# Kernel tuning notes

Measured on AMD Instinct MI355X. Metric: run time of the kernel, lower is better.

The kernel has to match this reference:

```python
import jax, jax.numpy as jnp
import numpy as np

T, B, D, H = 1024, 64, 1024, 30  # seq_len, batch, input_size, hidden_size


def setup_inputs() -> dict:
    key = jax.random.key(0)
    ks = jax.random.split(key, 11)
    sc = 1.0 / np.sqrt(H)  # torch default init scale ~ U(-1/sqrt(H), 1/sqrt(H))
    u = lambda k, shape: jax.random.uniform(k, shape, dtype=jnp.float32, minval=-sc, maxval=sc)
    return {
        "x": jax.random.normal(ks[0], (T, B, D), dtype=jnp.float32),
        "W_ih0": u(ks[1], (4 * H, D)),
        "W_hh0": u(ks[2], (4 * H, H)),
        "b_ih0": u(ks[3], (4 * H,)),
        "b_hh0": u(ks[4], (4 * H,)),
        "W_ih1": u(ks[5], (4 * H, H)),
        "W_hh1": u(ks[6], (4 * H, H)),
        "b_ih1": u(ks[7], (4 * H,)),
        "b_hh1": u(ks[8], (4 * H,)),
        "W_out": u(ks[9], (1, H)),
        "b_out": u(ks[10], (1,)),
    }


def _lstm_layer(xs, Wih, Whh, bih, bhh):
    # xs: [T, B, Din] -> hs: [T, B, H]. PyTorch gate order: i, f, g, o.
    xg = jnp.einsum("tbd,gd->tbg", xs, Wih) + (bih + bhh)  # precompute input projection
    h0 = jnp.zeros((xs.shape[1], H), xs.dtype)
    c0 = jnp.zeros((xs.shape[1], H), xs.dtype)

    def step(carry, xw):
        h, c = carry
        gates = xw + h @ Whh.T  # [B, 4H]
        i, f, g, o = jnp.split(gates, 4, axis=-1)
        c = jax.nn.sigmoid(f) * c + jax.nn.sigmoid(i) * jnp.tanh(g)
        h = jax.nn.sigmoid(o) * jnp.tanh(c)
        return (h, c), h

    _, hs = jax.lax.scan(step, (h0, c0), xg)
    return hs


def reference(x, W_ih0, W_hh0, b_ih0, b_hh0, W_ih1, W_hh1, b_ih1, b_hh1, W_out, b_out):
    h1 = _lstm_layer(x, W_ih0, W_hh0, b_ih0, b_hh0)   # layer 0
    h2 = _lstm_layer(h1, W_ih1, W_hh1, b_ih1, b_hh1)  # layer 1
    return h2 @ W_out.T + b_out  # [T, B, 1]
```

## Files before the change

kernel.cpp:

```cpp
#include <hip/hip_runtime.h>
#include <hip/hip_bf16.h>
#include <cstdint>

#define TT 1024
#define BB 64
#define DD 1024
#define HH 30
#define G4 120
#define KC 16

__device__ __forceinline__ float frcp(float x) { return __builtin_amdgcn_rcpf(x); }
__device__ __forceinline__ float fsig(float x) { return frcp(1.0f + __expf(-x)); }
__device__ __forceinline__ float ftan(float x) {
    return 2.0f * frcp(1.0f + __expf(-2.0f * x)) - 1.0f;
}
__device__ __forceinline__ float bcast(float v, int l) {
    return __int_as_float(__builtin_amdgcn_readlane(__float_as_int(v), l));
}

__global__ void prep_kernel(const float* __restrict__ Wih0,
                            const float* __restrict__ bih0,
                            const float* __restrict__ bhh0,
                            float* __restrict__ Wt0, float* __restrict__ bias0) {
    int idx = blockIdx.x * 256 + threadIdx.x;
    int k = idx >> 7, g = idx & 127;
    Wt0[idx] = (g < G4) ? Wih0[g * DD + k] : 0.0f;
    if (idx < 128) bias0[idx] = (idx < G4) ? (bih0[idx] + bhh0[idx]) : 0.0f;
}

__global__ __launch_bounds__(256) void gemm_xg(
    const float* __restrict__ x, const float* __restrict__ Wt0,
    const float* __restrict__ bias0, float* __restrict__ xgp) {
    __shared__ __align__(16) float xs[KC][136];
    __shared__ __align__(16) float ws[KC][132];
    const int tid = threadIdx.x;
    const int r0 = blockIdx.x * 128;
    const int rg = tid >> 4;
    const int cg = tid & 15;

    const int sr = tid >> 1;
    const int sk = (tid & 1) * 8;
    const int ka = tid >> 5;
    const int ca = (tid & 31) * 4;

    float acc[8][8];
#pragma unroll
    for (int i = 0; i < 8; ++i)
#pragma unroll
        for (int j = 0; j < 8; ++j) acc[i][j] = 0.0f;

    const float* xrow = x + (size_t)(r0 + sr) * DD;
    float4 px0 = *(const float4*)&xrow[sk];
    float4 px1 = *(const float4*)&xrow[sk + 4];
    float4 pw0 = *(const float4*)&Wt0[(size_t)ka * 128 + ca];
    float4 pw1 = *(const float4*)&Wt0[(size_t)(ka + 8) * 128 + ca];

    for (int kc = 0; kc < DD / KC; ++kc) {
        __syncthreads();
        xs[sk + 0][sr] = px0.x; xs[sk + 1][sr] = px0.y;
        xs[sk + 2][sr] = px0.z; xs[sk + 3][sr] = px0.w;
        xs[sk + 4][sr] = px1.x; xs[sk + 5][sr] = px1.y;
        xs[sk + 6][sr] = px1.z; xs[sk + 7][sr] = px1.w;
        *(float4*)&ws[ka][ca]     = pw0;
        *(float4*)&ws[ka + 8][ca] = pw1;
        __syncthreads();

        if (kc + 1 < DD / KC) {
            const int k0 = (kc + 1) * KC;
            px0 = *(const float4*)&xrow[k0 + sk];
            px1 = *(const float4*)&xrow[k0 + sk + 4];
            pw0 = *(const float4*)&Wt0[(size_t)(k0 + ka) * 128 + ca];
            pw1 = *(const float4*)&Wt0[(size_t)(k0 + ka + 8) * 128 + ca];
        }

#pragma unroll
        for (int kk = 0; kk < KC; ++kk) {
            float4 xa = *(const float4*)&xs[kk][rg * 8];
            float4 xb = *(const float4*)&xs[kk][rg * 8 + 4];
            float4 wa = *(const float4*)&ws[kk][cg * 8];
            float4 wb = *(const float4*)&ws[kk][cg * 8 + 4];
            float xr[8] = {xa.x, xa.y, xa.z, xa.w, xb.x, xb.y, xb.z, xb.w};
            float wr[8] = {wa.x, wa.y, wa.z, wa.w, wb.x, wb.y, wb.z, wb.w};
#pragma unroll
            for (int i = 0; i < 8; ++i)
#pragma unroll
                for (int j = 0; j < 8; ++j)
                    acc[i][j] = fmaf(xr[i], wr[j], acc[i][j]);
        }
    }

#pragma unroll
    for (int j = 0; j < 8; ++j) {
        const int g = cg * 8 + j;
        if (g < G4) {
            const int gm = g % 60;
            const int lane = (gm < HH) ? gm : (32 + gm - HH);
            const int slot = g / 60;
            const float bb = bias0[g];
#pragma unroll
            for (int i = 0; i < 8; ++i) {
                const size_t row = r0 + rg * 8 + i;
                xgp[(row * 64 + lane) * 2 + slot] = acc[i][j] + bb;
            }
        }
    }
}

__global__ __launch_bounds__(64, 1) void lstm_rec(
    const float* __restrict__ xgp,
    const float* __restrict__ Whh0, const float* __restrict__ Wih1,
    const float* __restrict__ Whh1, const float* __restrict__ bih1,
    const float* __restrict__ bhh1, float* __restrict__ h2buf) {
    const int l = threadIdx.x;
    const int b = blockIdx.x;
    const int u = l & 31;
    const int half = l >> 5;
    const bool act = (u < HH);
    const int rlo = half * HH + (act ? u : 0);
    const int rhi = 60 + rlo;

    float w0lo[HH], w0hi[HH], wi1lo[HH], wi1hi[HH], wh1lo[HH], wh1hi[HH];
#pragma unroll
    for (int j = 0; j < HH; ++j) {
        w0lo[j]  = act ? Whh0[rlo * HH + j] : 0.0f;
        w0hi[j]  = act ? Whh0[rhi * HH + j] : 0.0f;
        wi1lo[j] = act ? Wih1[rlo * HH + j] : 0.0f;
        wi1hi[j] = act ? Wih1[rhi * HH + j] : 0.0f;
        wh1lo[j] = act ? Whh1[rlo * HH + j] : 0.0f;
        wh1hi[j] = act ? Whh1[rhi * HH + j] : 0.0f;
    }
    const float b1lo = act ? (bih1[rlo] + bhh1[rlo]) : 0.0f;
    const float b1hi = act ? (bih1[rhi] + bhh1[rhi]) : 0.0f;

    float h1 = 0.0f, c1 = 0.0f, h2 = 0.0f, c2 = 0.0f;
    float hb1[HH], hb2[HH];
#pragma unroll
    for (int j = 0; j < HH; ++j) { hb1[j] = 0.0f; hb2[j] = 0.0f; }

    const float2* xgptr = (const float2*)xgp + (size_t)b * 64 + l;
    float2 xq[4];
#pragma unroll
    for (int p = 0; p < 4; ++p) xq[p] = xgptr[(size_t)p * (BB * 64)];

    for (int t = 0; t < TT; t += 4) {
#pragma unroll
        for (int p = 0; p < 4; ++p) {
            const int tc = t + p;
            const float2 xw = xq[p];
            const int tn = (tc + 4 < TT) ? tc + 4 : TT - 1;
            xq[p] = xgptr[(size_t)tn * (BB * 64)];

            float aA = xw.x, aB = 0.0f, bA = xw.y, bB = 0.0f;
#pragma unroll
            for (int j = 0; j < HH; j += 2) {
                aA = fmaf(w0lo[j], hb1[j], aA);
                bA = fmaf(w0hi[j], hb1[j], bA);
                aB = fmaf(w0lo[j + 1], hb1[j + 1], aB);
                bB = fmaf(w0hi[j + 1], hb1[j + 1], bB);
            }
            const float alo = aA + aB, ahi = bA + bB;
            const float plo = __shfl_xor(alo, 32, 64);
            const float phi = __shfl_xor(ahi, 32, 64);

            float zA = b1lo, zB = 0.0f, yA = b1hi, yB = 0.0f;
#pragma unroll
            for (int j = 0; j < HH; j += 2) {
                zA = fmaf(wh1lo[j], hb2[j], zA);
                yA = fmaf(wh1hi[j], hb2[j], yA);
                zB = fmaf(wh1lo[j + 1], hb2[j + 1], zB);
                yB = fmaf(wh1hi[j + 1], hb2[j + 1], yB);
            }

            float ipre = half ? plo : alo;
            float fpre = half ? alo : plo;
            float gpre = half ? phi : ahi;
            float opre = half ? ahi : phi;
            c1 = fsig(fpre) * c1 + fsig(ipre) * ftan(gpre);
            h1 = fsig(opre) * ftan(c1);

#pragma unroll
            for (int j = 0; j < HH; ++j) hb1[j] = bcast(h1, j);

#pragma unroll
            for (int j = 0; j < HH; j += 2) {
                zA = fmaf(wi1lo[j], hb1[j], zA);
                yA = fmaf(wi1hi[j], hb1[j], yA);
                zB = fmaf(wi1lo[j + 1], hb1[j + 1], zB);
                yB = fmaf(wi1hi[j + 1], hb1[j + 1], yB);
            }
            const float zlo = zA + zB, zhi = yA + yB;
            const float qlo = __shfl_xor(zlo, 32, 64);
            const float qhi = __shfl_xor(zhi, 32, 64);

            ipre = half ? qlo : zlo;
            fpre = half ? zlo : qlo;
            gpre = half ? qhi : zhi;
            opre = half ? zhi : qhi;
            c2 = fsig(fpre) * c2 + fsig(ipre) * ftan(gpre);
            h2 = fsig(opre) * ftan(c2);

            if (l < HH) h2buf[((size_t)tc * BB + b) * 32 + l] = h2;

#pragma unroll
            for (int j = 0; j < HH; ++j) hb2[j] = bcast(h2, j);
        }
    }
}

__global__ __launch_bounds__(256) void out_proj(
    const float* __restrict__ h2buf, const float* __restrict__ Wout,
    const float* __restrict__ bout, float* __restrict__ out) {
    __shared__ float wos[32];
    if (threadIdx.x < 32)
        wos[threadIdx.x] = (threadIdx.x < HH) ? Wout[threadIdx.x] : 0.0f;
    __syncthreads();
    const int idx = blockIdx.x * 256 + threadIdx.x;
    const float4* hp = (const float4*)(h2buf + (size_t)idx * 32);
    float s0 = 0.f, s1 = 0.f;
#pragma unroll
    for (int q = 0; q < 8; ++q) {
        float4 h = hp[q];
        s0 = fmaf(h.x, wos[q * 4 + 0], s0);
        s1 = fmaf(h.y, wos[q * 4 + 1], s1);
        s0 = fmaf(h.z, wos[q * 4 + 2], s0);
        s1 = fmaf(h.w, wos[q * 4 + 3], s1);
    }
    out[idx] = s0 + s1 + bout[0];
}

extern "C" void kernel_launch(void* const* d_in, const int* in_sizes, int n_in,
                              void* d_out, int out_size, void* d_ws, size_t ws_size,
                              hipStream_t stream) {
    const float* x    = (const float*)d_in[0];
    const float* Wih0 = (const float*)d_in[1];
    const float* Whh0 = (const float*)d_in[2];
    const float* bih0 = (const float*)d_in[3];
    const float* bhh0 = (const float*)d_in[4];
    const float* Wih1 = (const float*)d_in[5];
    const float* Whh1 = (const float*)d_in[6];
    const float* bih1 = (const float*)d_in[7];
    const float* bhh1 = (const float*)d_in[8];
    const float* Wout = (const float*)d_in[9];
    const float* bout = (const float*)d_in[10];
    float* out = (float*)d_out;

    char* ws = (char*)d_ws;
    float* Wt0   = (float*)ws;
    float* bias0 = (float*)(ws + 512 * 1024);
    float* xgp   = (float*)(ws + 1024 * 1024);
    float* h2buf = (float*)(ws + 36 * 1024 * 1024);

    prep_kernel<<<512, 256, 0, stream>>>(Wih0, bih0, bhh0, Wt0, bias0);
    gemm_xg<<<512, 256, 0, stream>>>(x, Wt0, bias0, xgp);
    lstm_rec<<<BB, 64, 0, stream>>>(xgp, Whh0, Wih1, Whh1, bih1, bhh1, h2buf);
    out_proj<<<256, 256, 0, stream>>>(h2buf, Wout, bout, out);
}
```

Before: 1.206 ms.

## Use split-bf16 MFMA for input GEMM and pipeline LSTM layers across two waves

The fp32 SIMT input-projection GEMM becomes an MFMA bf16x3 scheme, with hi/lo bf16 splits of x and the weights prepacked into MFMA fragment layout, so matrix cores do the large GEMM while keeping near-fp32 accuracy. The recurrent kernel now runs two wavefronts per batch element: wave 0 runs layer 0 and the layer-1 input projection, and wave 1 runs layer 1 one timestep behind, exchanging partial gates through double-buffered shared memory. This shortens the serial per-step critical path at the cost of a __syncthreads every step and some truncation error from the bf16 split of x.

Measured after the change: 1.063 ms. -11.8%, faster.

```diff
diff --git a/kernel.cpp b/kernel.cpp
--- a/kernel.cpp
+++ b/kernel.cpp
@@ -7,7 +7,9 @@
 #define DD 1024
 #define HH 30
 #define G4 120
-#define KC 16
+
+typedef __attribute__((ext_vector_type(8))) short short8;
+typedef __attribute__((ext_vector_type(4))) float float4v;
 
 __device__ __forceinline__ float frcp(float x) { return __builtin_amdgcn_rcpf(x); }
 __device__ __forceinline__ float fsig(float x) { return frcp(1.0f + __expf(-x)); }
@@ -17,193 +19,232 @@
 __device__ __forceinline__ float bcast(float v, int l) {
     return __int_as_float(__builtin_amdgcn_readlane(__float_as_int(v), l));
 }
+__device__ __forceinline__ unsigned short bf16_rne(float f) {
+    unsigned u = __float_as_uint(f);
+    return (unsigned short)((u + 0x7FFFu + ((u >> 16) & 1u)) >> 16);
+}
 
 __global__ void prep_kernel(const float* __restrict__ Wih0,
                             const float* __restrict__ bih0,
                             const float* __restrict__ bhh0,
-                            float* __restrict__ Wt0, float* __restrict__ bias0) {
+                            unsigned short* __restrict__ Bhi,
+                            unsigned short* __restrict__ Blo,
+                            float* __restrict__ bias0) {
     int idx = blockIdx.x * 256 + threadIdx.x;
-    int k = idx >> 7, g = idx & 127;
-    Wt0[idx] = (g < G4) ? Wih0[g * DD + k] : 0.0f;
+    int l  = idx & 63;
+    int kc = (idx >> 6) & 31;
+    int nt = idx >> 11;
+    int n = nt * 16 + (l & 15);
+    int kb = kc * 32 + (l >> 4) * 8;
+    size_t o = (size_t)idx * 8;
+#pragma unroll
+    for (int j = 0; j < 8; ++j) {
+        float wv = (n < G4) ? Wih0[(size_t)n * DD + kb + j] : 0.0f;
+        unsigned short hi = bf16_rne(wv);
+        float fhi = __uint_as_float((unsigned)hi << 16);
+        unsigned short lo = bf16_rne(wv - fhi);
+        Bhi[o + j] = hi;
+        Blo[o + j] = lo;
+    }
     if (idx < 128) bias0[idx] = (idx < G4) ? (bih0[idx] + bhh0[idx]) : 0.0f;
 }
 
 __global__ __launch_bounds__(256) void gemm_xg(
-    const float* __restrict__ x, const float* __restrict__ Wt0,
-    const float* __restrict__ bias0, float* __restrict__ xgp) {
-    __shared__ __align__(16) float xs[KC][136];
-    __shared__ __align__(16) float ws[KC][132];
+    const float* __restrict__ x, const unsigned short* __restrict__ Bhi,
+    const unsigned short* __restrict__ Blo, const float* __restrict__ bias0,
+    float* __restrict__ xgp) {
     const int tid = threadIdx.x;
-    const int r0 = blockIdx.x * 128;
-    const int rg = tid >> 4;
-    const int cg = tid & 15;
-
-    const int sr = tid >> 1;
-    const int sk = (tid & 1) * 8;
-    const int ka = tid >> 5;
-    const int ca = (tid & 31) * 4;
-
-    float acc[8][8];
-#pragma unroll
-    for (int i = 0; i < 8; ++i)
-#pragma unroll
-        for (int j = 0; j < 8; ++j) acc[i][j] = 0.0f;
-
-    const float* xrow = x + (size_t)(r0 + sr) * DD;
-    float4 px0 = *(const float4*)&xrow[sk];
-    float4 px1 = *(const float4*)&xrow[sk + 4];
-    float4 pw0 = *(const float4*)&Wt0[(size_t)ka * 128 + ca];
-    float4 pw1 = *(const float4*)&Wt0[(size_t)(ka + 8) * 128 + ca];
-
-    for (int kc = 0; kc < DD / KC; ++kc) {
-        __syncthreads();
-        xs[sk + 0][sr] = px0.x; xs[sk + 1][sr] = px0.y;
-        xs[sk + 2][sr] = px0.z; xs[sk + 3][sr] = px0.w;
-        xs[sk + 4][sr] = px1.x; xs[sk + 5][sr] = px1.y;
-        xs[sk + 6][sr] = px1.z; xs[sk + 7][sr] = px1.w;
-        *(float4*)&ws[ka][ca]     = pw0;
-        *(float4*)&ws[ka + 8][ca] = pw1;
-        __syncthreads();
-
-        if (kc + 1 < DD / KC) {
-            const int k0 = (kc + 1) * KC;
-            px0 = *(const float4*)&xrow[k0 + sk];
-            px1 = *(const float4*)&xrow[k0 + sk + 4];
-            pw0 = *(const float4*)&Wt0[(size_t)(k0 + ka) * 128 + ca];
-            pw1 = *(const float4*)&Wt0[(size_t)(k0 + ka + 8) * 128 + ca];
-        }
-
-#pragma unroll
-        for (int kk = 0; kk < KC; ++kk) {
-            float4 xa = *(const float4*)&xs[kk][rg * 8];
-            float4 xb = *(const float4*)&xs[kk][rg * 8 + 4];
-            float4 wa = *(const float4*)&ws[kk][cg * 8];
-            float4 wb = *(const float4*)&ws[kk][cg * 8 + 4];
-            float xr[8] = {xa.x, xa.y, xa.z, xa.w, xb.x, xb.y, xb.z, xb.w};
-            float wr[8] = {wa.x, wa.y, wa.z, wa.w, wb.x, wb.y, wb.z, wb.w};
-#pragma unroll
-            for (int i = 0; i < 8; ++i)
-#pragma unroll
-                for (int j = 0; j < 8; ++j)
-                    acc[i][j] = fmaf(xr[i], wr[j], acc[i][j]);
-        }
-    }
-
-#pragma unroll
-    for (int j = 0; j < 8; ++j) {
-        const int g = cg * 8 + j;
+    const int w = tid >> 6;
+    const int l = tid & 63;
+    const int lm = l & 15, lq = l >> 4;
+    const int r0 = blockIdx.x * 128 + w * 32;
+
+    float4v acc[2][8];
+#pragma unroll
+    for (int mt = 0; mt < 2; ++mt)
+#pragma unroll
+        for (int nt = 0; nt < 8; ++nt) acc[mt][nt] = (float4v)0.0f;
+
+    const float* aptr[2];
+    aptr[0] = x + (size_t)(r0 + lm) * DD + lq * 8;
+    aptr[1] = x + (size_t)(r0 + 16 + lm) * DD + lq * 8;
+
+    float4 pa[2][2];
+#pragma unroll
+    for (int mt = 0; mt < 2; ++mt) {
+        pa[mt][0] = *(const float4*)(aptr[mt]);
+        pa[mt][1] = *(const float4*)(aptr[mt] + 4);
+    }
+
+    for (int kc = 0; kc < 32; ++kc) {
+        short8 ahi[2], alo[2];
+#pragma unroll
+        for (int mt = 0; mt < 2; ++mt) {
+            float f[8] = {pa[mt][0].x, pa[mt][0].y, pa[mt][0].z, pa[mt][0].w,
+                          pa[mt][1].x, pa[mt][1].y, pa[mt][1].z, pa[mt][1].w};
+#pragma unroll
+            for (int i = 0; i < 8; ++i) {
+                unsigned ub = __float_as_uint(f[i]);
+                ahi[mt][i] = (short)(ub >> 16);
+                float fr = f[i] - __uint_as_float(ub & 0xFFFF0000u);
+                alo[mt][i] = (short)(__float_as_uint(fr) >> 16);
+            }
+        }
+        if (kc + 1 < 32) {
+            const int ko = (kc + 1) * 32;
+#pragma unroll
+            for (int mt = 0; mt < 2; ++mt) {
+                pa[mt][0] = *(const float4*)(aptr[mt] + ko);
+                pa[mt][1] = *(const float4*)(aptr[mt] + ko + 4);
+            }
+        }
+#pragma unroll
+        for (int nt = 0; nt < 8; ++nt) {
+            const size_t bo = ((size_t)(nt * 32 + kc) * 64 + l) * 8;
+            short8 bh = *(const short8*)(Bhi + bo);
+            short8 bl = *(const short8*)(Blo + bo);
+            acc[0][nt] = __builtin_amdgcn_mfma_f32_16x16x32_bf16(ahi[0], bh, acc[0][nt], 0, 0, 0);
+            acc[1][nt] = __builtin_amdgcn_mfma_f32_16x16x32_bf16(ahi[1], bh, acc[1][nt], 0, 0, 0);
+            acc[0][nt] = __builtin_amdgcn_mfma_f32_16x16x32_bf16(alo[0], bh, acc[0][nt], 0, 0, 0);
+            acc[1][nt] = __builtin_amdgcn_mfma_f32_16x16x32_bf16(alo[1], bh, acc[1][nt], 0, 0, 0);
+            acc[0][nt] = __builtin_amdgcn_mfma_f32_16x16x32_bf16(ahi[0], bl, acc[0][nt], 0, 0, 0);
+            acc[1][nt] = __builtin_amdgcn_mfma_f32_16x16x32_bf16(ahi[1], bl, acc[1][nt], 0, 0, 0);
+        }
+    }
+
+#pragma unroll
+    for (int nt = 0; nt < 8; ++nt) {
+        const int g = nt * 16 + lm;
         if (g < G4) {
             const int gm = g % 60;
-            const int lane = (gm < HH) ? gm : (32 + gm - HH);
+            const int lane_t = (gm < HH) ? gm : (32 + gm - HH);
             const int slot = g / 60;
             const float bb = bias0[g];
 #pragma unroll
-            for (int i = 0; i < 8; ++i) {
-                const size_t row = r0 + rg * 8 + i;
-                xgp[(row * 64 + lane) * 2 + slot] = acc[i][j] + bb;
-            }
-        }
-    }
-}
-
-__global__ __launch_bounds__(64, 1) void lstm_rec(
-    const float* __restrict__ xgp,
-    const float* __restrict__ Whh0, const float* __restrict__ Wih1,
-    const float* __restrict__ Whh1, const float* __restrict__ bih1,
-    const float* __restrict__ bhh1, float* __restrict__ h2buf) {
-    const int l = threadIdx.x;
+            for (int mt = 0; mt < 2; ++mt)
+#pragma unroll
+                for (int i = 0; i < 4; ++i) {
+                    const size_t row = r0 + mt * 16 + lq * 4 + i;
+                    xgp[(row * 64 + lane_t) * 2 + slot] = acc[mt][nt][i] + bb;
+                }
+        }
+    }
+}
+
+__global__ __launch_bounds__(128, 1) void lstm_rec(
+    const float* __restrict__ xgp, const float* __restrict__ Whh0,
+    const float* __restrict__ Wih1, const float* __restrict__ Whh1,
+    const float* __restrict__ bih1, const float* __restrict__ bhh1,
+    float* __restrict__ h2buf) {
+    const int tid = threadIdx.x;
+    const int wv = tid >> 6;
+    const int l = tid & 63;
     const int b = blockIdx.x;
     const int u = l & 31;
     const int half = l >> 5;
-    const bool act = (u < HH);
-    const int rlo = half * HH + (act ? u : 0);
+    const bool al = (u < HH);
+    const int rlo = half * HH + (al ? u : 0);
     const int rhi = 60 + rlo;
 
-    float w0lo[HH], w0hi[HH], wi1lo[HH], wi1hi[HH], wh1lo[HH], wh1hi[HH];
-#pragma unroll
-    for (int j = 0; j < HH; ++j) {
-        w0lo[j]  = act ? Whh0[rlo * HH + j] : 0.0f;
-        w0hi[j]  = act ? Whh0[rhi * HH + j] : 0.0f;
-        wi1lo[j] = act ? Wih1[rlo * HH + j] : 0.0f;
-        wi1hi[j] = act ? Wih1[rhi * HH + j] : 0.0f;
-        wh1lo[j] = act ? Whh1[rlo * HH + j] : 0.0f;
-        wh1hi[j] = act ? Whh1[rhi * HH + j] : 0.0f;
-    }
-    const float b1lo = act ? (bih1[rlo] + bhh1[rlo]) : 0.0f;
-    const float b1hi = act ? (bih1[rhi] + bhh1[rhi]) : 0.0f;
-
-    float h1 = 0.0f, c1 = 0.0f, h2 = 0.0f, c2 = 0.0f;
-    float hb1[HH], hb2[HH];
-#pragma unroll
-    for (int j = 0; j < HH; ++j) { hb1[j] = 0.0f; hb2[j] = 0.0f; }
+    __shared__ float2 pg[2][64];
+
+    float wa[HH], wb[HH], wc[HH], wd[HH];
+    float b1lo = 0.f, b1hi = 0.f;
+    if (wv == 0) {
+#pragma unroll
+        for (int j = 0; j < HH; ++j) {
+            wa[j] = al ? Whh0[rlo * HH + j] : 0.f;
+            wb[j] = al ? Whh0[rhi * HH + j] : 0.f;
+            wc[j] = al ? Wih1[rlo * HH + j] : 0.f;
+            wd[j] = al ? Wih1[rhi * HH + j] : 0.f;
+        }
+        b1lo = al ? (bih1[rlo] + bhh1[rlo]) : 0.f;
+        b1hi = al ? (bih1[rhi] + bhh1[rhi]) : 0.f;
+    } else {
+#pragma unroll
+        for (int j = 0; j < HH; ++j) {
+            wa[j] = al ? Whh1[rlo * HH + j] : 0.f;
+            wb[j] = al ? Whh1[rhi * HH + j] : 0.f;
+            wc[j] = 0.f; wd[j] = 0.f;
+        }
+    }
+
+    float hstate = 0.f, cstate = 0.f;
+    float hb[HH];
+#pragma unroll
+    for (int j = 0; j < HH; ++j) hb[j] = 0.f;
 
     const float2* xgptr = (const float2*)xgp + (size_t)b * 64 + l;
     float2 xq[4];
-#pragma unroll
-    for (int p = 0; p < 4; ++p) xq[p] = xgptr[(size_t)p * (BB * 64)];
-
-    for (int t = 0; t < TT; t += 4) {
-#pragma unroll
-        for (int p = 0; p < 4; ++p) {
-            const int tc = t + p;
-            const float2 xw = xq[p];
-            const int tn = (tc + 4 < TT) ? tc + 4 : TT - 1;
-            xq[p] = xgptr[(size_t)tn * (BB * 64)];
-
-            float aA = xw.x, aB = 0.0f, bA = xw.y, bB = 0.0f;
-#pragma unroll
-            for (int j = 0; j < HH; j += 2) {
-                aA = fmaf(w0lo[j], hb1[j], aA);
-                bA = fmaf(w0hi[j], hb1[j], bA);
-                aB = fmaf(w0lo[j + 1], hb1[j + 1], aB);
-                bB = fmaf(w0hi[j + 1], hb1[j + 1], bB);
-            }
-            const float alo = aA + aB, ahi = bA + bB;
-            const float plo = __shfl_xor(alo, 32, 64);
-            const float phi = __shfl_xor(ahi, 32, 64);
-
-            float zA = b1lo, zB = 0.0f, yA = b1hi, yB = 0.0f;
-#pragma unroll
-            for (int j = 0; j < HH; j += 2) {
-                zA = fmaf(wh1lo[j], hb2[j], zA);
-                yA = fmaf(wh1hi[j], hb2[j], yA);
-                zB = fmaf(wh1lo[j + 1], hb2[j + 1], zB);
-                yB = fmaf(wh1hi[j + 1], hb2[j + 1], yB);
-            }
-
-            float ipre = half ? plo : alo;
-            float fpre = half ? alo : plo;
-            float gpre = half ? phi : ahi;
-            float opre = half ? ahi : phi;
-            c1 = fsig(fpre) * c1 + fsig(ipre) * ftan(gpre);
-            h1 = fsig(opre) * ftan(c1);
-
-#pragma unroll
-            for (int j = 0; j < HH; ++j) hb1[j] = bcast(h1, j);
-
-#pragma unroll
-            for (int j = 0; j < HH; j += 2) {
-                zA = fmaf(wi1lo[j], hb1[j], zA);
-                yA = fmaf(wi1hi[j], hb1[j], yA);
-                zB = fmaf(wi1lo[j + 1], hb1[j + 1], zB);
-                yB = fmaf(wi1hi[j + 1], hb1[j + 1], yB);
-            }
-            const float zlo = zA + zB, zhi = yA + yB;
-            const float qlo = __shfl_xor(zlo, 32, 64);
-            const float qhi = __shfl_xor(zhi, 32, 64);
-
-            ipre = half ? qlo : zlo;
-            fpre = half ? zlo : qlo;
-            gpre = half ? qhi : zhi;
-            opre = half ? zhi : qhi;
-            c2 = fsig(fpre) * c2 + fsig(ipre) * ftan(gpre);
-            h2 = fsig(opre) * ftan(c2);
-
-            if (l < HH) h2buf[((size_t)tc * BB + b) * 32 + l] = h2;
-
-#pragma unroll
-            for (int j = 0; j < HH; ++j) hb2[j] = bcast(h2, j);
-        }
+    if (wv == 0) {
+#pragma unroll
+        for (int p = 0; p < 4; ++p) xq[p] = xgptr[(size_t)p * (BB * 64)];
+    }
+
+    for (int t = 0; t <= TT; ++t) {
+        if (wv == 0) {
+            if (t < TT) {
+                float2 xw = xq[t & 3];
+                const int tn = (t + 4 < TT) ? t + 4 : TT - 1;
+                xq[t & 3] = xgptr[(size_t)tn * (BB * 64)];
+
+                float aA = xw.x, aB = 0.f, cA = xw.y, cB = 0.f;
+#pragma unroll
+                for (int j = 0; j < HH; j += 2) {
+                    aA = fmaf(wa[j], hb[j], aA);
+                    cA = fmaf(wb[j], hb[j], cA);
+                    aB = fmaf(wa[j + 1], hb[j + 1], aB);
+                    cB = fmaf(wb[j + 1], hb[j + 1], cB);
+                }
+                float alo = aA + aB, ahi = cA + cB;
+                float plo = __shfl_xor(alo, 32, 64);
+                float phi = __shfl_xor(ahi, 32, 64);
+                float ipre = half ? plo : alo;
+                float fpre = half ? alo : plo;
+                float gpre = half ? phi : ahi;
+                float opre = half ? ahi : phi;
+                cstate = fsig(fpre) * cstate + fsig(ipre) * ftan(gpre);
+                hstate = fsig(opre) * ftan(cstate);
+#pragma unroll
+                for (int j = 0; j < HH; ++j) hb[j] = bcast(hstate, j);
+
+                float zA = b1lo, zB = 0.f, yA = b1hi, yB = 0.f;
+#pragma unroll
+                for (int j = 0; j < HH; j += 2) {
+                    zA = fmaf(wc[j], hb[j], zA);
+                    yA = fmaf(wd[j], hb[j], yA);
+                    zB = fmaf(wc[j + 1], hb[j + 1], zB);
+                    yB = fmaf(wd[j + 1], hb[j + 1], yB);
+                }
+                pg[t & 1][l] = make_float2(zA + zB, yA + yB);
+            }
+        } else {
+            if (t > 0) {
+                const int s = t - 1;
+                float2 part = pg[s & 1][l];
+                float zA = part.x, zB = 0.f, yA = part.y, yB = 0.f;
+#pragma unroll
+                for (int j = 0; j < HH; j += 2) {
+                    zA = fmaf(wa[j], hb[j], zA);
+                    yA = fmaf(wb[j], hb[j], yA);
+                    zB = fmaf(wa[j + 1], hb[j + 1], zB);
+                    yB = fmaf(wb[j + 1], hb[j + 1], yB);
+                }
+                float zlo = zA + zB, zhi = yA + yB;
+                float qlo = __shfl_xor(zlo, 32, 64);
+                float qhi = __shfl_xor(zhi, 32, 64);
+                float ipre = half ? qlo : zlo;
+                float fpre = half ? zlo : qlo;
+                float gpre = half ? qhi : zhi;
+                float opre = half ? zhi : qhi;
+                cstate = fsig(fpre) * cstate + fsig(ipre) * ftan(gpre);
+                hstate = fsig(opre) * ftan(cstate);
+#pragma unroll
+                for (int j = 0; j < HH; ++j) hb[j] = bcast(hstate, j);
+                if (l < HH) h2buf[((size_t)s * BB + b) * 32 + l] = hstate;
+            }
+        }
+        __syncthreads();
     }
 }
 
@@ -245,13 +286,14 @@
     float* out = (float*)d_out;
 
     char* ws = (char*)d_ws;
-    float* Wt0   = (float*)ws;
-    float* bias0 = (float*)(ws + 512 * 1024);
+    unsigned short* Bhi = (unsigned short*)ws;
+    unsigned short* Blo = (unsigned short*)(ws + 262144);
+    float* bias0 = (float*)(ws + 524288);
     float* xgp   = (float*)(ws + 1024 * 1024);
     float* h2buf = (float*)(ws + 36 * 1024 * 1024);
 
-    prep_kernel<<<512, 256, 0, stream>>>(Wih0, bih0, bhh0, Wt0, bias0);
-    gemm_xg<<<512, 256, 0, stream>>>(x, Wt0, bias0, xgp);
-    lstm_rec<<<BB, 64, 0, stream>>>(xgp, Whh0, Wih1, Whh1, bih1, bhh1, h2buf);
+    prep_kernel<<<64, 256, 0, stream>>>(Wih0, bih0, bhh0, Bhi, Blo, bias0);
+    gemm_xg<<<512, 256, 0, stream>>>(x, Bhi, Blo, bias0, xgp);
+    lstm_rec<<<BB, 128, 0, stream>>>(xgp, Whh0, Wih1, Whh1, bih1, bhh1, h2buf);
     out_proj<<<256, 256, 0, stream>>>(h2buf, Wout, bout, out);
 }
```
